# Performance work log

Hardware: AMD Instinct MI355X
Metric: run time of the kernel (lower is better)

Reference implementation:

```python
import jax, jax.numpy as jnp
import numpy as np

B, S, D, FF, E, TOP_K = 4, 2048, 1024, 4096, 8, 2


def setup_inputs() -> dict:
    key = jax.random.key(0)
    ks = jax.random.split(key, 13)
    sd = 1.0 / np.sqrt(D)
    sf = 1.0 / np.sqrt(FF)
    return {
        "x":   jax.random.normal(ks[0], (B, S, D), jnp.float32),
        # parallel 2-way router
        "Wr":  jax.random.normal(ks[1], (D, 2), jnp.float32) * sd,
        "br":  jnp.zeros((2,), jnp.float32),
        # MoE gate
        "Wg":  jax.random.normal(ks[2], (D, E), jnp.float32) * sd,
        "bg":  jnp.zeros((E,), jnp.float32),
        # expert FFNs
        "W1":  jax.random.normal(ks[3], (E, D, FF), jnp.float32) * sd,
        "b1":  jnp.zeros((E, FF), jnp.float32),
        "W2":  jax.random.normal(ks[4], (E, FF, D), jnp.float32) * sf,
        "b2":  jnp.zeros((E, D), jnp.float32),
        # dense FFN
        "D1":  jax.random.normal(ks[5], (D, FF), jnp.float32) * sd,
        "d1b": jnp.zeros((FF,), jnp.float32),
        "D2":  jax.random.normal(ks[6], (FF, D), jnp.float32) * sf,
        "d2b": jnp.zeros((D,), jnp.float32),
    }


def _hybrid_moe(x, Wr, br, Wg, bg, W1, b1, W2, b2, D1, d1b, D2, d2b):
    b, s, d = x.shape
    t = x.reshape(-1, d)                                  # [T, D]
    T = t.shape[0]

    # parallel 2-way blend router
    rp = jax.nn.softmax(x @ Wr + br, axis=-1)             # [B, S, 2]

    # MoE gating: softmax over experts, top-k, renormalize
    gp = jax.nn.softmax(t @ Wg + bg, axis=-1)             # [T, E]
    vals, idx = jax.lax.top_k(gp, TOP_K)                  # [T, K]
    vals = vals / jnp.sum(vals, axis=-1, keepdims=True)
    cw = jnp.zeros((T, E), t.dtype).at[jnp.arange(T)[:, None], idx].add(vals)  # [T, E]

    # expert FFNs (ReLU MLP), combined with top-k weights
    h = jax.nn.relu(jnp.einsum('td,edf->tef', t, W1) + b1)       # [T, E, FF]
    eo = jnp.einsum('tef,efd->ted', h, W2) + b2                  # [T, E, D]
    moe = jnp.einsum('te,ted->td', cw, eo).reshape(b, s, d)

    # dense FFN branch
    dense = jax.nn.relu(x @ D1 + d1b) @ D2 + d2b

    return rp[..., 0:1] * moe + rp[..., 1:2] * dense


def reference(x, Wr, br, Wg, bg, W1, b1, W2, b2, D1, d1b, D2, d2b):
    return _hybrid_moe(x, Wr, br, Wg, bg, W1, b1, W2, b2, D1, d1b, D2, d2b)
```

## Files before the change

kernel.cpp:

```cpp
#include <hip/hip_runtime.h>
#include <stdint.h>

#define T_TOK   8192
#define D_DIM   1024
#define FF_DIM  4096
#define E_NUM   8
#define SLOT_MAX 18432
#define RT_MAX  104

typedef unsigned int   u32;
typedef unsigned short u16;
typedef __attribute__((ext_vector_type(4))) float  f32x4;
typedef __attribute__((ext_vector_type(4))) float  f4;
typedef __attribute__((ext_vector_type(8))) short  bf16x8;
typedef __attribute__((ext_vector_type(8))) unsigned short u16x8;
typedef __attribute__((ext_vector_type(4))) unsigned short u16x4;

__device__ __forceinline__ u16 f2bf(float f) {
  u32 u = __builtin_bit_cast(u32, f);
  return (u16)((u + 0x7fffu + ((u >> 16) & 1u)) >> 16);
}
__device__ __forceinline__ float bf2f(u16 h) {
  u32 u = ((u32)h) << 16; return __builtin_bit_cast(float, u);
}

typedef const __attribute__((address_space(1))) u32* gp1_t;
typedef __attribute__((address_space(3))) u32*       lp3_t;
__device__ __forceinline__ void gload16(const u16* g, u16* l) {
  __builtin_amdgcn_global_load_lds((gp1_t)(const void*)g, (lp3_t)l, 16, 0, 0);
}

__global__ __launch_bounds__(256) void k_route(
    const float* __restrict__ x, const float* __restrict__ Wr, const float* __restrict__ br,
    const float* __restrict__ Wg, const float* __restrict__ bg,
    int* __restrict__ hdr, int4* __restrict__ tok_sel, float4* __restrict__ tok_wf,
    u16* __restrict__ xb)
{
  int w = threadIdx.x >> 6, l = threadIdx.x & 63;
  int t = blockIdx.x * 4 + w;
  const float* xt = x + (size_t)t * D_DIM;
  u16* xbt = xb + (size_t)t * D_DIM;
  float p[10];
  #pragma unroll
  for (int i = 0; i < 10; ++i) p[i] = 0.f;
  #pragma unroll
  for (int j = 0; j < 4; ++j) {
    int d0 = j * 256 + l * 4;
    f4 xv = *(const f4*)&xt[d0];
    u16x4 xo; xo[0]=f2bf(xv[0]); xo[1]=f2bf(xv[1]); xo[2]=f2bf(xv[2]); xo[3]=f2bf(xv[3]);
    *(u16x4*)&xbt[d0] = xo;
    f4 wra = *(const f4*)&Wr[d0 * 2];
    f4 wrb = *(const f4*)&Wr[d0 * 2 + 4];
    p[0] += xv[0]*wra[0] + xv[1]*wra[2] + xv[2]*wrb[0] + xv[3]*wrb[2];
    p[1] += xv[0]*wra[1] + xv[1]*wra[3] + xv[2]*wrb[1] + xv[3]*wrb[3];
    #pragma unroll
    for (int i = 0; i < 4; ++i) {
      f4 g0 = *(const f4*)&Wg[(size_t)(d0 + i) * 8];
      f4 g1 = *(const f4*)&Wg[(size_t)(d0 + i) * 8 + 4];
      p[2] += xv[i]*g0[0]; p[3] += xv[i]*g0[1]; p[4] += xv[i]*g0[2]; p[5] += xv[i]*g0[3];
      p[6] += xv[i]*g1[0]; p[7] += xv[i]*g1[1]; p[8] += xv[i]*g1[2]; p[9] += xv[i]*g1[3];
    }
  }
  #pragma unroll
  for (int off = 32; off; off >>= 1) {
    #pragma unroll
    for (int i = 0; i < 10; ++i) p[i] += __shfl_xor(p[i], off, 64);
  }
  if (l == 0) {
    float a0 = p[0] + br[0], a1 = p[1] + br[1];
    float m  = fmaxf(a0, a1);
    float e0 = __expf(a0 - m), e1 = __expf(a1 - m);
    float rs = 1.f / (e0 + e1);
    float rp0 = e0 * rs, rp1 = e1 * rs;
    float g[E_NUM]; float gm = -1e30f;
    #pragma unroll
    for (int e = 0; e < E_NUM; ++e) { g[e] = p[2 + e] + bg[e]; gm = fmaxf(gm, g[e]); }
    int i0 = 0;
    #pragma unroll
    for (int e = 1; e < E_NUM; ++e) if (g[e] > g[i0]) i0 = e;
    int i1 = (i0 == 0) ? 1 : 0;
    #pragma unroll
    for (int e = 0; e < E_NUM; ++e) if (e != i0 && g[e] > g[i1]) i1 = e;
    float x0 = __expf(g[i0] - gm), x1 = __expf(g[i1] - gm);
    float s = 1.f / (x0 + x1);
    int r0 = atomicAdd(&hdr[i0], 1);
    int r1 = atomicAdd(&hdr[i1], 1);
    tok_sel[t] = make_int4(i0, r0, i1, r1);
    tok_wf[t]  = make_float4(x0 * s, x1 * s, rp0, rp1);
  }
}

__global__ __launch_bounds__(256) void k_setup(
    int* __restrict__ hdr, int4* __restrict__ tilemap, int* __restrict__ perm,
    const int4* __restrict__ tok_sel, int2* __restrict__ tok_slot)
{
  __shared__ int soff[E_NUM + 1];
  int tid = threadIdx.x;
  if (tid == 0) {
    int acc = 0;
    for (int e = 0; e < E_NUM; ++e) {
      soff[e] = acc; hdr[8 + e] = acc;
      acc += (hdr[e] + 255) & ~255;
    }
    soff[E_NUM] = acc;
    hdr[16] = acc;
    hdr[17] = acc >> 8;
    hdr[18] = (acc >> 8) + T_TOK / 256;
  }
  __syncthreads();
  int nmoe = soff[E_NUM] >> 8;
  for (int rt = tid; rt < RT_MAX; rt += 256) {
    int4 ent;
    if (rt < nmoe) {
      int row0 = rt * 256;
      int e = 0;
      while (e < E_NUM - 1 && row0 >= soff[e + 1]) ++e;
      ent = make_int4(0, row0, e, 0);
    } else if (rt < nmoe + T_TOK / 256) {
      ent = make_int4(1, (rt - nmoe) * 256, -1, 0);
    } else {
      ent = make_int4(-1, 0, 0, 0);
    }
    tilemap[rt] = ent;
  }
  for (int s = tid; s < SLOT_MAX; s += 256) perm[s] = -1;
  __syncthreads();
  for (int t = tid; t < T_TOK; t += 256) {
    int4 s = tok_sel[t];
    int s0 = soff[s.x] + s.y;
    int s1 = soff[s.z] + s.w;
    perm[s0] = t; perm[s1] = t;
    tok_slot[t] = make_int2(s0, s1);
  }
}

__global__ __launch_bounds__(256) void k_tcast_all(
    const float* __restrict__ W1, const float* __restrict__ W2,
    const float* __restrict__ D1, const float* __restrict__ D2,
    u16* __restrict__ W1bt, u16* __restrict__ W2bt,
    u16* __restrict__ D1bt, u16* __restrict__ D2bt)
{
  int bid = blockIdx.x;
  int panel = bid >> 10, pb = bid & 1023;
  const float* s; u16* d; int R, C, ltc;
  if (panel < 8)       { s = W1 + (size_t)panel * D_DIM * FF_DIM; d = W1bt + (size_t)panel * D_DIM * FF_DIM; R = D_DIM;  C = FF_DIM; ltc = 6; }
  else if (panel < 16) { int e = panel - 8;
                         s = W2 + (size_t)e * FF_DIM * D_DIM;     d = W2bt + (size_t)e * FF_DIM * D_DIM;     R = FF_DIM; C = D_DIM;  ltc = 4; }
  else if (panel == 16){ s = D1; d = D1bt; R = D_DIM;  C = FF_DIM; ltc = 6; }
  else                 { s = D2; d = D2bt; R = FF_DIM; C = D_DIM;  ltc = 4; }
  int tc = pb & ((1 << ltc) - 1), tr = pb >> ltc;

  __shared__ float tile[64][65];
  int t = threadIdx.x;
  #pragma unroll
  for (int p = 0; p < 4; ++p) {
    int r = p * 16 + (t >> 4);
    int c4 = (t & 15) * 4;
    f4 v = *(const f4*)&s[(size_t)(tr * 64 + r) * C + tc * 64 + c4];
    tile[r][c4+0] = v[0]; tile[r][c4+1] = v[1]; tile[r][c4+2] = v[2]; tile[r][c4+3] = v[3];
  }
  __syncthreads();
  #pragma unroll
  for (int q = 0; q < 2; ++q) {
    int oc = q * 32 + (t >> 3);
    int r8 = (t & 7) * 8;
    u16x8 o;
    #pragma unroll
    for (int j = 0; j < 8; ++j) o[j] = f2bf(tile[r8 + j][oc]);
    *(u16x8*)&d[(size_t)(tc * 64 + oc) * R + tr * 64 + r8] = o;
  }
}

#define LGKM0() { asm volatile("s_waitcnt lgkmcnt(0)" ::: "memory"); \
                  __builtin_amdgcn_sched_barrier(0); }
#define BAR()   __builtin_amdgcn_s_barrier()

template <int RELU, int GATHER>
__global__ __launch_bounds__(512, 2) void k_gemm8p(
    const u16* __restrict__ Amoe, const u16* __restrict__ Aden,
    const u16* __restrict__ Bexp, const u16* __restrict__ Bden,
    const float* __restrict__ biasexp, const float* __restrict__ biasden,
    u16* __restrict__ Omoe, u16* __restrict__ Oden,
    const int* __restrict__ hdr, const int4* __restrict__ tilemap,
    const int* __restrict__ perm,
    int K, int N, long bexp_stride, int biasexp_stride, int lg2gx)
{
  int gx  = 1 << lg2gx;
  int nwg = gx * gridDim.y;
  int lin = blockIdx.y * gx + blockIdx.x;
  int sw  = (lin & 7) * (nwg >> 3) + (lin >> 3);
  int ct  = sw & (gx - 1);
  int rt  = sw >> lg2gx;
  if (rt >= hdr[18]) return;

  int4 ent = tilemap[rt];
  const u16* B; const float* bias; u16* O;
  if (ent.x == 1) { B = Bden; bias = biasden; O = Oden; }
  else {
    B = Bexp + (size_t)ent.z * bexp_stride;
    bias = biasexp + (size_t)ent.z * biasexp_stride;
    O = Omoe;
  }
  const int row0 = ent.y;

  __shared__ __align__(16) u16 lds[65536];

  const int tid = threadIdx.x;
  const int wid = tid >> 6, l = tid & 63;
  const int wm = wid >> 2, wn = wid & 3;

  const int srow = wid * 8 + (l >> 3);
  const int skel = ((l & 7) ^ (l >> 3)) * 8;
  const u16* aSrcP[4];
  const u16* bSrcP[4];
  #pragma unroll
  for (int i = 0; i < 4; ++i) {
    int r = srow + i * 64;
    if (ent.x == 1)      aSrcP[i] = Aden + (size_t)(row0 + r) * K + skel;
    else if (GATHER) {
      int pr = perm[row0 + r]; pr = pr < 0 ? 0 : pr;
      aSrcP[i] = Amoe + (size_t)pr * K + skel;
    } else               aSrcP[i] = Amoe + (size_t)(row0 + r) * K + skel;
    bSrcP[i] = B + (size_t)(ct * 256 + r) * K + skel;
  }

  const int fr = l & 15, fq = l >> 4;
  const int fx = (l & 7) << 4;
  const int cs0 = (fq * 16) ^ fx;
  const int cs1 = (64 + fq * 16) ^ fx;
  const int brow = (wn & 1) * 64;
  const char* ldsc = (const char*)lds;
  const char* aP0 = ldsc + wm * 16384 + fr * 128 + cs0;
  const char* aP1 = ldsc + wm * 16384 + fr * 128 + cs1;
  const char* bP0 = ldsc + 65536 + (wn >> 1) * 16384 + (brow + fr) * 128 + cs0;
  const char* bP1 = ldsc + 65536 + (wn >> 1) * 16384 + (brow + fr) * 128 + cs1;

  auto STAGE_A = [&](int tt, int h, int bb) {
    u16* dst = &lds[(bb * 2 + h) * 8192 + wid * 512];
    gload16(aSrcP[h * 2]     + tt * 64, dst);
    gload16(aSrcP[h * 2 + 1] + tt * 64, dst + 4096);
  };
  auto STAGE_B = [&](int tt, int h, int bb) {
    u16* dst = &lds[32768 + (bb * 2 + h) * 8192 + wid * 512];
    gload16(bSrcP[h * 2]     + tt * 64, dst);
    gload16(bSrcP[h * 2 + 1] + tt * 64, dst + 4096);
  };

  f32x4 acc[8][4];
  #pragma unroll
  for (int m = 0; m < 8; ++m)
    #pragma unroll
    for (int n = 0; n < 4; ++n) acc[m][n] = (f32x4){0.f, 0.f, 0.f, 0.f};

  bf16x8 a0[4][2], a1[4][2], b0[2][2], b1[2][2];

  #define READ_A0(B_) { _Pragma("unroll") for (int j = 0; j < 4; ++j) { \
      a0[j][0] = *(const bf16x8*)(aP0 + ((B_)*32768 + j*2048)); \
      a0[j][1] = *(const bf16x8*)(aP1 + ((B_)*32768 + j*2048)); } }
  #define READ_A1(B_) { _Pragma("unroll") for (int j = 0; j < 4; ++j) { \
      a1[j][0] = *(const bf16x8*)(aP0 + ((B_)*32768 + 8192 + j*2048)); \
      a1[j][1] = *(const bf16x8*)(aP1 + ((B_)*32768 + 8192 + j*2048)); } }
  #define READ_B0(B_) { _Pragma("unroll") for (int i = 0; i < 2; ++i) { \
      b0[i][0] = *(const bf16x8*)(bP0 + ((B_)*32768 + i*2048)); \
      b0[i][1] = *(const bf16x8*)(bP1 + ((B_)*32768 + i*2048)); } }
  #define READ_B1(B_) { _Pragma("unroll") for (int i = 0; i < 2; ++i) { \
      b1[i][0] = *(const bf16x8*)(bP0 + ((B_)*32768 + 4096 + i*2048)); \
      b1[i][1] = *(const bf16x8*)(bP1 + ((B_)*32768 + 4096 + i*2048)); } }
  #define MFMA_Q(am, bm, mo, no) { __builtin_amdgcn_s_setprio(1); \
    _Pragma("unroll") for (int j = 0; j < 4; ++j) \
      _Pragma("unroll") for (int i = 0; i < 2; ++i) { \
        acc[(mo) + j][(no) + i] = __builtin_amdgcn_mfma_f32_16x16x32_bf16(am[j][0], bm[i][0], acc[(mo) + j][(no) + i], 0, 0, 0); \
        acc[(mo) + j][(no) + i] = __builtin_amdgcn_mfma_f32_16x16x32_bf16(am[j][1], bm[i][1], acc[(mo) + j][(no) + i], 0, 0, 0); } \
    __builtin_amdgcn_s_setprio(0); }

  const int NK = K >> 6;

  STAGE_B(0, 0, 0); STAGE_B(0, 1, 0); STAGE_A(0, 0, 0); STAGE_A(0, 1, 0);
  STAGE_B(1, 0, 1); STAGE_B(1, 1, 1); STAGE_A(1, 0, 1);
  asm volatile("s_waitcnt vmcnt(6)" ::: "memory");
  BAR();

  #define TILE(B_, t_) { \
     \
    READ_A0(B_); READ_B0(B_); \
    if ((t_) + 1 < NK) STAGE_A((t_) + 1, 1, (B_) ^ 1); \
    BAR(); LGKM0(); \
    MFMA_Q(a0, b0, 0, 0); \
    BAR(); \
     \
    READ_B1(B_); \
    BAR(); LGKM0(); \
    MFMA_Q(a0, b1, 0, 2); \
    BAR(); \
     \
    READ_A1(B_); \
    if ((t_) + 2 < NK) STAGE_B((t_) + 2, 0, (B_)); \
    BAR(); LGKM0(); \
    MFMA_Q(a1, b1, 4, 2); \
    BAR(); \
     \
    if ((t_) + 2 < NK) { STAGE_B((t_) + 2, 1, (B_)); STAGE_A((t_) + 2, 0, (B_)); } \
    BAR(); \
    MFMA_Q(a1, b0, 4, 0); \
    if ((t_) < NK - 2) { asm volatile("s_waitcnt vmcnt(6)" ::: "memory"); } \
    else               { asm volatile("s_waitcnt vmcnt(0)" ::: "memory"); } \
    BAR(); \
    __builtin_amdgcn_sched_barrier(0); }

  for (int t = 0; t < NK; t += 2) {
    TILE(0, t);
    TILE(1, t + 1);
  }
  #undef TILE

  __syncthreads();
  float bv[4];
  #pragma unroll
  for (int ni = 0; ni < 4; ++ni) bv[ni] = bias[ct * 256 + wn * 64 + ni * 16 + fr];
  float* ep = (float*)((char*)lds + wid * 4608);
  const int row16 = l >> 2, cg = l & 3;
  #pragma unroll
  for (int mi = 0; mi < 8; ++mi) {
    #pragma unroll
    for (int ni = 0; ni < 4; ++ni) {
      f32x4 v = acc[mi][ni];
      #pragma unroll
      for (int j = 0; j < 4; ++j) {
        float f = v[j] + bv[ni];
        if (RELU) f = fmaxf(f, 0.f);
        ep[(fq * 4 + j) * 68 + ni * 16 + fr] = f;
      }
    }
    #pragma unroll
    for (int p = 0; p < 2; ++p) {
      f4 r0 = *(f4*)&ep[row16 * 68 + (cg + p * 4) * 8];
      f4 r1 = *(f4*)&ep[row16 * 68 + (cg + p * 4) * 8 + 4];
      u16x8 o;
      o[0]=f2bf(r0[0]); o[1]=f2bf(r0[1]); o[2]=f2bf(r0[2]); o[3]=f2bf(r0[3]);
      o[4]=f2bf(r1[0]); o[5]=f2bf(r1[1]); o[6]=f2bf(r1[2]); o[7]=f2bf(r1[3]);
      int rr = row0 + wm * 128 + mi * 16 + row16;
      int cc = ct * 256 + wn * 64 + (cg + p * 4) * 8;
      *(u16x8*)&O[(size_t)rr * N + cc] = o;
    }
  }
  #undef READ_A0
  #undef READ_A1
  #undef READ_B0
  #undef READ_B1
  #undef MFMA_Q
}

__global__ __launch_bounds__(128) void k_combine(
    const u16* __restrict__ eo, const u16* __restrict__ dense_o,
    const float4* __restrict__ tok_wf, const int2* __restrict__ tok_slot,
    float* __restrict__ out)
{
  int t = blockIdx.x;
  int c8 = threadIdx.x;
  float4 wf = tok_wf[t];
  int2 sl = tok_slot[t];
  u16x8 a  = *((const u16x8*)(eo + (size_t)sl.x * D_DIM) + c8);
  u16x8 b  = *((const u16x8*)(eo + (size_t)sl.y * D_DIM) + c8);
  u16x8 dn = *((const u16x8*)(dense_o + (size_t)t * D_DIM) + c8);
  float* op = out + (size_t)t * D_DIM + c8 * 8;
  #pragma unroll
  for (int j = 0; j < 8; ++j) {
    float mo = wf.x * bf2f(a[j]) + wf.y * bf2f(b[j]);
    op[j] = wf.z * mo + wf.w * bf2f(dn[j]);
  }
}

extern "C" void kernel_launch(void* const* d_in, const int* in_sizes, int n_in,
                              void* d_out, int out_size, void* d_ws, size_t ws_size,
                              hipStream_t stream)
{
  const float* x   = (const float*)d_in[0];
  const float* Wr  = (const float*)d_in[1];
  const float* br  = (const float*)d_in[2];
  const float* Wg  = (const float*)d_in[3];
  const float* bg  = (const float*)d_in[4];
  const float* W1  = (const float*)d_in[5];
  const float* b1  = (const float*)d_in[6];
  const float* W2  = (const float*)d_in[7];
  const float* b2  = (const float*)d_in[8];
  const float* D1  = (const float*)d_in[9];
  const float* d1b = (const float*)d_in[10];
  const float* D2  = (const float*)d_in[11];
  const float* d2b = (const float*)d_in[12];
  float* out = (float*)d_out;

  char* base = (char*)d_ws;
  size_t cur = 0;
  auto alloc = [&](size_t b) -> void* {
    void* p = base + cur; cur = (cur + b + 255) & ~(size_t)255; return p;
  };
  int*    hdr      = (int*)   alloc(256 * sizeof(int));
  int4*   tilemap  = (int4*)  alloc((size_t)RT_MAX * sizeof(int4));
  int4*   tok_sel  = (int4*)  alloc((size_t)T_TOK * sizeof(int4));
  float4* tok_wf   = (float4*)alloc((size_t)T_TOK * sizeof(float4));
  int2*   tok_slot = (int2*)  alloc((size_t)T_TOK * sizeof(int2));
  int*    perm     = (int*)   alloc((size_t)SLOT_MAX * sizeof(int));
  u16*    xb       = (u16*)   alloc((size_t)T_TOK * D_DIM * 2);
  u16*    W1bt     = (u16*)   alloc((size_t)E_NUM * D_DIM * FF_DIM * 2);
  u16*    W2bt     = (u16*)   alloc((size_t)E_NUM * D_DIM * FF_DIM * 2);
  u16*    D1bt     = (u16*)   alloc((size_t)D_DIM * FF_DIM * 2);
  u16*    D2bt     = (u16*)   alloc((size_t)D_DIM * FF_DIM * 2);
  u16*    h_moe    = (u16*)   alloc((size_t)SLOT_MAX * FF_DIM * 2);
  u16*    h_dense  = (u16*)   alloc((size_t)T_TOK * FF_DIM * 2);
  u16*    eo       = (u16*)   alloc((size_t)SLOT_MAX * D_DIM * 2);
  u16*    dense_o  = (u16*)   alloc((size_t)T_TOK * D_DIM * 2);
  (void)in_sizes; (void)n_in; (void)out_size; (void)ws_size;

  hipMemsetAsync(hdr, 0, 256 * sizeof(int), stream);
  k_route    <<<T_TOK / 4, 256, 0, stream>>>(x, Wr, br, Wg, bg, hdr, tok_sel, tok_wf, xb);
  k_setup    <<<1, 256, 0, stream>>>(hdr, tilemap, perm, tok_sel, tok_slot);
  k_tcast_all<<<18 * 1024, 256, 0, stream>>>(W1, W2, D1, D2, W1bt, W2bt, D1bt, D2bt);

  k_gemm8p<1, 1><<<dim3(FF_DIM / 256, RT_MAX), 512, 0, stream>>>(
      xb, xb, W1bt, D1bt, b1, d1b, h_moe, h_dense, hdr, tilemap, perm,
      D_DIM, FF_DIM, (long)D_DIM * FF_DIM, FF_DIM, 4);
  k_gemm8p<0, 0><<<dim3(D_DIM / 256, RT_MAX), 512, 0, stream>>>(
      h_moe, h_dense, W2bt, D2bt, b2, d2b, eo, dense_o, hdr, tilemap, perm,
      FF_DIM, D_DIM, (long)D_DIM * FF_DIM, D_DIM, 2);

  k_combine<<<T_TOK, 128, 0, stream>>>(eo, dense_o, tok_wf, tok_slot, out);
}
```

Baseline: 780.5 us.

## Parallelize setup kernel, enlarge transpose-cast tiles, reschedule GEMM B-staging

The setup kernel now runs on 32 blocks instead of one: each thread recomputes the expert offsets redundantly, and only the padding slots of perm are cleared rather than the whole array. The weight transpose-cast kernel handles 128x64 tiles per block, halving the block count and doubling each block's LDS tile. The GEMM main loop issues the B-tile global staging loads one sub-step earlier and adds a partial lgkmcnt wait, spreading global loads more evenly across the MFMA phases. These changes target serial setup latency, launch overhead in the cast, and load/compute overlap in the GEMMs. The larger LDS tile may lower cast-kernel occupancy.

Measured after the change: 757.9 us. 2.9% less time.

```diff
diff --git a/kernel.cpp b/kernel.cpp
--- a/kernel.cpp
+++ b/kernel.cpp
@@ -94,22 +94,26 @@
     int* __restrict__ hdr, int4* __restrict__ tilemap, int* __restrict__ perm,
     const int4* __restrict__ tok_sel, int2* __restrict__ tok_slot)
 {
-  __shared__ int soff[E_NUM + 1];
-  int tid = threadIdx.x;
-  if (tid == 0) {
-    int acc = 0;
-    for (int e = 0; e < E_NUM; ++e) {
-      soff[e] = acc; hdr[8 + e] = acc;
-      acc += (hdr[e] + 255) & ~255;
-    }
-    soff[E_NUM] = acc;
+  int soff[E_NUM + 1], cnt[E_NUM];
+  int acc = 0;
+  #pragma unroll
+  for (int e = 0; e < E_NUM; ++e) {
+    cnt[e] = hdr[e];
+    soff[e] = acc;
+    acc += (cnt[e] + 255) & ~255;
+  }
+  soff[E_NUM] = acc;
+  const int gtid = blockIdx.x * 256 + threadIdx.x;
+  const int nthr = gridDim.x * 256;
+  if (gtid == 0) {
+    #pragma unroll
+    for (int e = 0; e < E_NUM; ++e) hdr[8 + e] = soff[e];
     hdr[16] = acc;
     hdr[17] = acc >> 8;
     hdr[18] = (acc >> 8) + T_TOK / 256;
   }
-  __syncthreads();
-  int nmoe = soff[E_NUM] >> 8;
-  for (int rt = tid; rt < RT_MAX; rt += 256) {
+  int nmoe = acc >> 8;
+  for (int rt = gtid; rt < RT_MAX; rt += nthr) {
     int4 ent;
     if (rt < nmoe) {
       int row0 = rt * 256;
@@ -123,9 +127,13 @@
     }
     tilemap[rt] = ent;
   }
-  for (int s = tid; s < SLOT_MAX; s += 256) perm[s] = -1;
-  __syncthreads();
-  for (int t = tid; t < T_TOK; t += 256) {
+  #pragma unroll
+  for (int e = 0; e < E_NUM; ++e) {
+    int lo = soff[e] + cnt[e];
+    int hi = soff[e + 1];
+    for (int s = lo + gtid; s < hi; s += nthr) perm[s] = -1;
+  }
+  for (int t = gtid; t < T_TOK; t += nthr) {
     int4 s = tok_sel[t];
     int s0 = soff[s.x] + s.y;
     int s1 = soff[s.z] + s.w;
@@ -141,7 +149,7 @@
     u16* __restrict__ D1bt, u16* __restrict__ D2bt)
 {
   int bid = blockIdx.x;
-  int panel = bid >> 10, pb = bid & 1023;
+  int panel = bid >> 9, pb = bid & 511;
   const float* s; u16* d; int R, C, ltc;
   if (panel < 8)       { s = W1 + (size_t)panel * D_DIM * FF_DIM; d = W1bt + (size_t)panel * D_DIM * FF_DIM; R = D_DIM;  C = FF_DIM; ltc = 6; }
   else if (panel < 16) { int e = panel - 8;
@@ -150,24 +158,24 @@
   else                 { s = D2; d = D2bt; R = FF_DIM; C = D_DIM;  ltc = 4; }
   int tc = pb & ((1 << ltc) - 1), tr = pb >> ltc;
 
-  __shared__ float tile[64][65];
+  __shared__ float tile[128][65];
   int t = threadIdx.x;
   #pragma unroll
-  for (int p = 0; p < 4; ++p) {
+  for (int p = 0; p < 8; ++p) {
     int r = p * 16 + (t >> 4);
     int c4 = (t & 15) * 4;
-    f4 v = *(const f4*)&s[(size_t)(tr * 64 + r) * C + tc * 64 + c4];
+    f4 v = *(const f4*)&s[(size_t)(tr * 128 + r) * C + tc * 64 + c4];
     tile[r][c4+0] = v[0]; tile[r][c4+1] = v[1]; tile[r][c4+2] = v[2]; tile[r][c4+3] = v[3];
   }
   __syncthreads();
   #pragma unroll
-  for (int q = 0; q < 2; ++q) {
-    int oc = q * 32 + (t >> 3);
-    int r8 = (t & 7) * 8;
+  for (int q = 0; q < 4; ++q) {
+    int oc = q * 16 + (t >> 4);
+    int r8 = (t & 15) * 8;
     u16x8 o;
     #pragma unroll
     for (int j = 0; j < 8; ++j) o[j] = f2bf(tile[r8 + j][oc]);
-    *(u16x8*)&d[(size_t)(tc * 64 + oc) * R + tr * 64 + r8] = o;
+    *(u16x8*)&d[(size_t)(tc * 64 + oc) * R + tr * 128 + r8] = o;
   }
 }
 
@@ -284,22 +292,24 @@
      \
     READ_A0(B_); READ_B0(B_); \
     if ((t_) + 1 < NK) STAGE_A((t_) + 1, 1, (B_) ^ 1); \
+    asm volatile("s_waitcnt lgkmcnt(8)" ::: "memory"); \
     BAR(); LGKM0(); \
     MFMA_Q(a0, b0, 0, 0); \
     BAR(); \
      \
     READ_B1(B_); \
+    if ((t_) + 2 < NK) STAGE_B((t_) + 2, 0, (B_)); \
     BAR(); LGKM0(); \
     MFMA_Q(a0, b1, 0, 2); \
     BAR(); \
      \
     READ_A1(B_); \
-    if ((t_) + 2 < NK) STAGE_B((t_) + 2, 0, (B_)); \
+    if ((t_) + 2 < NK) STAGE_B((t_) + 2, 1, (B_)); \
     BAR(); LGKM0(); \
     MFMA_Q(a1, b1, 4, 2); \
     BAR(); \
      \
-    if ((t_) + 2 < NK) { STAGE_B((t_) + 2, 1, (B_)); STAGE_A((t_) + 2, 0, (B_)); } \
+    if ((t_) + 2 < NK) STAGE_A((t_) + 2, 0, (B_)); \
     BAR(); \
     MFMA_Q(a1, b0, 4, 0); \
     if ((t_) < NK - 2) { asm volatile("s_waitcnt vmcnt(6)" ::: "memory"); } \
@@ -413,8 +423,8 @@
 
   hipMemsetAsync(hdr, 0, 256 * sizeof(int), stream);
   k_route    <<<T_TOK / 4, 256, 0, stream>>>(x, Wr, br, Wg, bg, hdr, tok_sel, tok_wf, xb);
-  k_setup    <<<1, 256, 0, stream>>>(hdr, tilemap, perm, tok_sel, tok_slot);
-  k_tcast_all<<<18 * 1024, 256, 0, stream>>>(W1, W2, D1, D2, W1bt, W2bt, D1bt, D2bt);
+  k_setup    <<<32, 256, 0, stream>>>(hdr, tilemap, perm, tok_sel, tok_slot);
+  k_tcast_all<<<18 * 512, 256, 0, stream>>>(W1, W2, D1, D2, W1bt, W2bt, D1bt, D2bt);
 
   k_gemm8p<1, 1><<<dim3(FF_DIM / 256, RT_MAX), 512, 0, stream>>>(
       xb, xb, W1bt, D1bt, b1, d1b, h_moe, h_dense, hdr, tilemap, perm,
```
